# Kernel tuning notes

Hardware: AMD Instinct MI355X
Metric: run time of the kernel (lower is better)

The kernel has to match this reference:

```python
import jax, jax.numpy as jnp
import numpy as np

N = 50000
E = 800000
IN_F = 64
OUT_F = 64
EDGE_F = 16


def setup_inputs() -> dict:
    key = jax.random.key(0)
    ks = jax.random.split(key, 8)
    x = jax.random.normal(ks[0], (N, IN_F), dtype=jnp.float32)
    edge_index = jax.random.randint(ks[1], (2, E), 0, N, dtype=jnp.int64)
    edge_attr = jax.random.normal(ks[2], (E, EDGE_F), dtype=jnp.float32)
    # MLP params: Linear(2*IN_F+EDGE_F -> OUT_F), ReLU, Linear(OUT_F -> OUT_F)
    d_in = 2 * IN_F + EDGE_F
    s1 = 1.0 / np.sqrt(d_in)
    s2 = 1.0 / np.sqrt(OUT_F)
    W1 = jax.random.uniform(ks[3], (d_in, OUT_F), minval=-s1, maxval=s1, dtype=jnp.float32)
    b1 = jax.random.uniform(ks[4], (OUT_F,), minval=-s1, maxval=s1, dtype=jnp.float32)
    W2 = jax.random.uniform(ks[5], (OUT_F, OUT_F), minval=-s2, maxval=s2, dtype=jnp.float32)
    b2 = jax.random.uniform(ks[6], (OUT_F,), minval=-s2, maxval=s2, dtype=jnp.float32)
    return {"x": x, "edge_index": edge_index, "edge_attr": edge_attr,
            "W1": W1, "b1": b1, "W2": W2, "b2": b2}


def reference(x, edge_index, edge_attr, W1, b1, W2, b2):
    src, dst = edge_index[0], edge_index[1]
    # gather source/target node features, concat with edge features: (E, 2*IN_F+EDGE_F)
    msg_in = jnp.concatenate([x[src], x[dst], edge_attr], axis=-1)
    h = jax.nn.relu(msg_in @ W1 + b1)
    msg = h @ W2 + b2                      # (E, OUT_F)
    # scatter-sum messages to destination nodes: (N, OUT_F)
    out = jax.ops.segment_sum(msg, dst, num_segments=N)
    return out
```

## Files before the change

kernel.cpp:

```cpp
#include <hip/hip_runtime.h>

#define N_NODES 50000
#define N_EDGES 800000

__global__ __launch_bounds__(256) void pre_kernel(
    const float* __restrict__ x, const float* __restrict__ W1,
    float* __restrict__ xa, float* __restrict__ xb)
{
    const int w = threadIdx.x >> 6;
    const int j = threadIdx.x & 63;
    const int gw = blockIdx.x * 4 + w;
    const int p = gw & 1;
    const int pair = gw >> 1;
    const int npair = (gridDim.x * 4) >> 1;

    float wc[64];
#pragma unroll
    for (int k = 0; k < 64; ++k) wc[k] = W1[(p * 64 + k) * 64 + j];

    float* __restrict__ outp = p ? xb : xa;

    for (int i = pair; i < N_NODES; i += npair) {
        const float4* xr = (const float4*)&x[(long)i * 64];
        float acc = 0.f;
#pragma unroll
        for (int k4 = 0; k4 < 16; ++k4) {
            float4 xv = xr[k4];
            acc += xv.x * wc[k4 * 4 + 0];
            acc += xv.y * wc[k4 * 4 + 1];
            acc += xv.z * wc[k4 * 4 + 2];
            acc += xv.w * wc[k4 * 4 + 3];
        }
        outp[(long)i * 64 + j] = acc;
    }
}

__global__ __launch_bounds__(256) void edge_kernel(
    const float* __restrict__ xa, const float* __restrict__ xb,
    const int* __restrict__ ei,
    const float* __restrict__ edge_attr,
    const float* __restrict__ W1, const float* __restrict__ b1,
    const float* __restrict__ W2, const float* __restrict__ b2,
    float* __restrict__ out)
{
    __shared__ __align__(16) float eas[4][256];
    __shared__ __align__(16) float hs[4][16][64];

    const int w = threadIdx.x >> 6;
    const int j = threadIdx.x & 63;
    const int wt = blockIdx.x * 4 + w;
    const long eb = (long)wt * 16;

    float w1c[16];
    float w2c[64];
#pragma unroll
    for (int k = 0; k < 16; ++k) w1c[k] = W1[(128 + k) * 64 + j];
#pragma unroll
    for (int k = 0; k < 64; ++k) w2c[k] = W2[k * 64 + j];
    const float b1j = b1[j];
    const float b2j = b2[j];

    int idxv = 0;
    if (j < 16)       idxv = ei[eb + j];
    else if (j < 32)  idxv = ei[(long)N_EDGES + eb + (j - 16)];

    {
        float4 ev = *(const float4*)&edge_attr[eb * 16 + j * 4];
        *(float4*)&eas[w][j * 4] = ev;
    }

#pragma unroll 4
    for (int e = 0; e < 16; ++e) {
        const int s  = __shfl(idxv, e);
        const int dd = __shfl(idxv, 16 + e);

        float acc = xa[(long)s * 64 + j] + xb[(long)dd * 64 + j] + b1j;
#pragma unroll
        for (int k4 = 0; k4 < 4; ++k4) {
            float4 ev = *(const float4*)&eas[w][e * 16 + k4 * 4];
            acc += ev.x * w1c[k4 * 4 + 0];
            acc += ev.y * w1c[k4 * 4 + 1];
            acc += ev.z * w1c[k4 * 4 + 2];
            acc += ev.w * w1c[k4 * 4 + 3];
        }
        const float h = fmaxf(acc, 0.f);
        hs[w][e][j] = h;

        float msg = b2j;
#pragma unroll
        for (int k4 = 0; k4 < 16; ++k4) {
            float4 hv = *(const float4*)&hs[w][e][k4 * 4];
            msg += hv.x * w2c[k4 * 4 + 0];
            msg += hv.y * w2c[k4 * 4 + 1];
            msg += hv.z * w2c[k4 * 4 + 2];
            msg += hv.w * w2c[k4 * 4 + 3];
        }
        unsafeAtomicAdd(&out[(long)dd * 64 + j], msg);
    }
}

__global__ __launch_bounds__(256) void fallback_kernel(
    const float* __restrict__ x, const int* __restrict__ ei,
    const float* __restrict__ edge_attr,
    const float* __restrict__ W1, const float* __restrict__ b1,
    const float* __restrict__ W2, const float* __restrict__ b2,
    float* __restrict__ out)
{
    const int w = threadIdx.x >> 6;
    const int j = threadIdx.x & 63;
    const long e = (long)blockIdx.x * 4 + w;
    if (e >= N_EDGES) return;
    const int s  = ei[e];
    const int dd = ei[(long)N_EDGES + e];

    float acc = b1[j];
    for (int k = 0; k < 64; ++k) acc += x[(long)s  * 64 + k] * W1[k * 64 + j];
    for (int k = 0; k < 64; ++k) acc += x[(long)dd * 64 + k] * W1[(64 + k) * 64 + j];
    for (int k = 0; k < 16; ++k) acc += edge_attr[e * 16 + k] * W1[(128 + k) * 64 + j];
    const float h = fmaxf(acc, 0.f);

    float msg = b2[j];
    for (int k = 0; k < 64; ++k) msg += __shfl(h, k) * W2[k * 64 + j];
    unsafeAtomicAdd(&out[(long)dd * 64 + j], msg);
}

extern "C" void kernel_launch(void* const* d_in, const int* in_sizes, int n_in,
                              void* d_out, int out_size, void* d_ws, size_t ws_size,
                              hipStream_t stream) {
    const float* x   = (const float*)d_in[0];
    const int*   ei  = (const int*)d_in[1];
    const float* ea  = (const float*)d_in[2];
    const float* W1  = (const float*)d_in[3];
    const float* b1  = (const float*)d_in[4];
    const float* W2  = (const float*)d_in[5];
    const float* b2  = (const float*)d_in[6];
    float* out = (float*)d_out;

    hipMemsetAsync(out, 0, (size_t)N_NODES * 64 * sizeof(float), stream);

    const size_t need = (size_t)2 * N_NODES * 64 * sizeof(float);
    if (ws_size >= need) {
        float* xauf = (float*)d_ws;
        float* xbuf = xauf + (size_t)N_NODES * 64;
        pre_kernel<<<512, 256, 0, stream>>>(x, W1, xauf, xbuf);
        edge_kernel<<<N_EDGES / 64, 256, 0, stream>>>(xauf, xbuf, ei, ea,
                                                      W1, b1, W2, b2, out);
    } else {
        fallback_kernel<<<N_EDGES / 4, 256, 0, stream>>>(x, ei, ea,
                                                         W1, b1, W2, b2, out);
    }
}
```

Measured before the change: 346.7 us.

## Use bf16 MFMA for per-edge MLP with persistent wave tiles

```diff
diff --git a/kernel.cpp b/kernel.cpp
--- a/kernel.cpp
+++ b/kernel.cpp
@@ -2,6 +2,15 @@
 
 #define N_NODES 50000
 #define N_EDGES 800000
+
+typedef __attribute__((ext_vector_type(8))) short bf16x8;
+typedef __attribute__((ext_vector_type(4))) float f32x4;
+
+__device__ inline short f2bf(float f) {
+    union { float f; unsigned u; } v; v.f = f;
+    unsigned r = v.u + 0x7FFFu + ((v.u >> 16) & 1u);
+    return (short)(r >> 16);
+}
 
 __global__ __launch_bounds__(256) void pre_kernel(
     const float* __restrict__ x, const float* __restrict__ W1,
@@ -22,20 +31,20 @@
 
     for (int i = pair; i < N_NODES; i += npair) {
         const float4* xr = (const float4*)&x[(long)i * 64];
-        float acc = 0.f;
+        float a0 = 0.f, a1 = 0.f, a2 = 0.f, a3 = 0.f;
 #pragma unroll
         for (int k4 = 0; k4 < 16; ++k4) {
             float4 xv = xr[k4];
-            acc += xv.x * wc[k4 * 4 + 0];
-            acc += xv.y * wc[k4 * 4 + 1];
-            acc += xv.z * wc[k4 * 4 + 2];
-            acc += xv.w * wc[k4 * 4 + 3];
-        }
-        outp[(long)i * 64 + j] = acc;
-    }
-}
-
-__global__ __launch_bounds__(256) void edge_kernel(
+            a0 += xv.x * wc[k4 * 4 + 0];
+            a1 += xv.y * wc[k4 * 4 + 1];
+            a2 += xv.z * wc[k4 * 4 + 2];
+            a3 += xv.w * wc[k4 * 4 + 3];
+        }
+        outp[(long)i * 64 + j] = (a0 + a1) + (a2 + a3);
+    }
+}
+
+__global__ __launch_bounds__(256) void edge_mfma(
     const float* __restrict__ xa, const float* __restrict__ xb,
     const int* __restrict__ ei,
     const float* __restrict__ edge_attr,
@@ -43,59 +52,101 @@
     const float* __restrict__ W2, const float* __restrict__ b2,
     float* __restrict__ out)
 {
-    __shared__ __align__(16) float eas[4][256];
-    __shared__ __align__(16) float hs[4][16][64];
+    __shared__ __align__(16) unsigned short hbuf[4][16][72];
 
     const int w = threadIdx.x >> 6;
-    const int j = threadIdx.x & 63;
-    const int wt = blockIdx.x * 4 + w;
-    const long eb = (long)wt * 16;
-
-    float w1c[16];
-    float w2c[64];
-#pragma unroll
-    for (int k = 0; k < 16; ++k) w1c[k] = W1[(128 + k) * 64 + j];
-#pragma unroll
-    for (int k = 0; k < 64; ++k) w2c[k] = W2[k * 64 + j];
-    const float b1j = b1[j];
-    const float b2j = b2[j];
-
-    int idxv = 0;
-    if (j < 16)       idxv = ei[eb + j];
-    else if (j < 32)  idxv = ei[(long)N_EDGES + eb + (j - 16)];
-
-    {
-        float4 ev = *(const float4*)&edge_attr[eb * 16 + j * 4];
-        *(float4*)&eas[w][j * 4] = ev;
-    }
-
-#pragma unroll 4
-    for (int e = 0; e < 16; ++e) {
-        const int s  = __shfl(idxv, e);
-        const int dd = __shfl(idxv, 16 + e);
-
-        float acc = xa[(long)s * 64 + j] + xb[(long)dd * 64 + j] + b1j;
-#pragma unroll
-        for (int k4 = 0; k4 < 4; ++k4) {
-            float4 ev = *(const float4*)&eas[w][e * 16 + k4 * 4];
-            acc += ev.x * w1c[k4 * 4 + 0];
-            acc += ev.y * w1c[k4 * 4 + 1];
-            acc += ev.z * w1c[k4 * 4 + 2];
-            acc += ev.w * w1c[k4 * 4 + 3];
-        }
-        const float h = fmaxf(acc, 0.f);
-        hs[w][e][j] = h;
-
-        float msg = b2j;
-#pragma unroll
-        for (int k4 = 0; k4 < 16; ++k4) {
-            float4 hv = *(const float4*)&hs[w][e][k4 * 4];
-            msg += hv.x * w2c[k4 * 4 + 0];
-            msg += hv.y * w2c[k4 * 4 + 1];
-            msg += hv.z * w2c[k4 * 4 + 2];
-            msg += hv.w * w2c[k4 * 4 + 3];
-        }
-        unsafeAtomicAdd(&out[(long)dd * 64 + j], msg);
+    const int l = threadIdx.x & 63;
+    const int n = l & 15;
+    const int q = l >> 4;
+
+    bf16x8 w1f[4];
+    bf16x8 w2f[4][2];
+    float b1v[4], b2v[4];
+#pragma unroll
+    for (int t = 0; t < 4; ++t) {
+        const int col = t * 16 + n;
+#pragma unroll
+        for (int i = 0; i < 8; ++i) {
+            const int k = q * 8 + i;
+            w1f[t][i] = (q < 2) ? f2bf(W1[(128 + k) * 64 + col]) : (short)0;
+            w2f[t][0][i] = f2bf(W2[k * 64 + col]);
+            w2f[t][1][i] = f2bf(W2[(32 + k) * 64 + col]);
+        }
+        b1v[t] = b1[col];
+        b2v[t] = b2[col];
+    }
+
+    const int nwaves = gridDim.x * 4;
+    const int gw = blockIdx.x * 4 + w;
+
+    for (int tile = gw; tile < N_EDGES / 16; tile += nwaves) {
+        const long eb = (long)tile * 16;
+
+        int idxv = 0;
+        if (l < 16)       idxv = ei[eb + l];
+        else if (l < 32)  idxv = ei[(long)N_EDGES + eb + (l - 16)];
+
+        int srcr[4], dstr[4];
+#pragma unroll
+        for (int r = 0; r < 4; ++r) {
+            srcr[r] = __shfl(idxv, q * 4 + r);
+            dstr[r] = __shfl(idxv, 16 + q * 4 + r);
+        }
+
+        bf16x8 eaf;
+        if (q < 2) {
+            const float* ep = &edge_attr[(eb + n) * 16 + q * 8];
+            float4 e0 = *(const float4*)ep;
+            float4 e1 = *(const float4*)(ep + 4);
+            eaf[0] = f2bf(e0.x); eaf[1] = f2bf(e0.y);
+            eaf[2] = f2bf(e0.z); eaf[3] = f2bf(e0.w);
+            eaf[4] = f2bf(e1.x); eaf[5] = f2bf(e1.y);
+            eaf[6] = f2bf(e1.z); eaf[7] = f2bf(e1.w);
+        } else {
+#pragma unroll
+            for (int i = 0; i < 8; ++i) eaf[i] = (short)0;
+        }
+
+        f32x4 c1[4];
+#pragma unroll
+        for (int t = 0; t < 4; ++t) {
+            f32x4 z = {0.f, 0.f, 0.f, 0.f};
+            c1[t] = __builtin_amdgcn_mfma_f32_16x16x32_bf16(eaf, w1f[t], z, 0, 0, 0);
+        }
+
+        float g[4][4];
+#pragma unroll
+        for (int t = 0; t < 4; ++t)
+#pragma unroll
+            for (int r = 0; r < 4; ++r)
+                g[t][r] = xa[(long)srcr[r] * 64 + t * 16 + n]
+                        + xb[(long)dstr[r] * 64 + t * 16 + n];
+
+#pragma unroll
+        for (int t = 0; t < 4; ++t)
+#pragma unroll
+            for (int r = 0; r < 4; ++r) {
+                float h = fmaxf(c1[t][r] + g[t][r] + b1v[t], 0.f);
+                hbuf[w][q * 4 + r][t * 16 + n] = (unsigned short)f2bf(h);
+            }
+
+        bf16x8 hf0 = *(const bf16x8*)&hbuf[w][n][q * 8];
+        bf16x8 hf1 = *(const bf16x8*)&hbuf[w][n][32 + q * 8];
+
+        f32x4 c2[4];
+#pragma unroll
+        for (int t = 0; t < 4; ++t) {
+            f32x4 z = {0.f, 0.f, 0.f, 0.f};
+            c2[t] = __builtin_amdgcn_mfma_f32_16x16x32_bf16(hf0, w2f[t][0], z, 0, 0, 0);
+            c2[t] = __builtin_amdgcn_mfma_f32_16x16x32_bf16(hf1, w2f[t][1], c2[t], 0, 0, 0);
+        }
+
+#pragma unroll
+        for (int t = 0; t < 4; ++t)
+#pragma unroll
+            for (int r = 0; r < 4; ++r)
+                unsafeAtomicAdd(&out[(long)dstr[r] * 64 + t * 16 + n],
+                                c2[t][r] + b2v[t]);
     }
 }
 
@@ -142,9 +193,9 @@
     if (ws_size >= need) {
         float* xauf = (float*)d_ws;
         float* xbuf = xauf + (size_t)N_NODES * 64;
-        pre_kernel<<<512, 256, 0, stream>>>(x, W1, xauf, xbuf);
-        edge_kernel<<<N_EDGES / 64, 256, 0, stream>>>(xauf, xbuf, ei, ea,
-                                                      W1, b1, W2, b2, out);
+        pre_kernel<<<1024, 256, 0, stream>>>(x, W1, xauf, xbuf);
+        edge_mfma<<<1024, 256, 0, stream>>>(xauf, xbuf, ei, ea,
+                                            W1, b1, W2, b2, out);
     } else {
         fallback_kernel<<<N_EDGES / 4, 256, 0, stream>>>(x, ei, ea,
                                                          W1, b1, W2, b2, out);
```

Measured after the change: 374.1 us. 7.9% more time.
